# Kernel optimization log

Hardware: AMD Instinct MI355X
Metric: run time of the kernel (lower is better)

## Reference

```python
import jax, jax.numpy as jnp
import numpy as np

IN_FEATURES = 4096
OUT_FEATURES = 4096
N_GROUPS = 32
GROUP_SIZE = IN_FEATURES // N_GROUPS  # 128


def setup_inputs() -> dict:
    key = jax.random.key(0)
    k_x, k_qw, k_s, k_zp, k_b = jax.random.split(key, 5)
    x = jax.random.normal(k_x, (2, 2048, IN_FEATURES), dtype=jnp.float32)
    # 4-bit GPTQ quantized weight values in [0, 16)
    qweight_int = jax.random.randint(k_qw, (IN_FEATURES, OUT_FEATURES), 0, 16, dtype=jnp.int32)
    scales = jax.random.uniform(k_s, (N_GROUPS, OUT_FEATURES), dtype=jnp.float32, minval=0.001, maxval=0.02)
    zero_points = jax.random.randint(k_zp, (N_GROUPS, OUT_FEATURES), 0, 16, dtype=jnp.int32)
    # standard (non-permuted) g_idx: group index per input channel
    g_idx = (jnp.arange(IN_FEATURES, dtype=jnp.int32) // GROUP_SIZE).astype(jnp.int32)
    bias = jax.random.normal(k_b, (OUT_FEATURES,), dtype=jnp.float32)
    return {"x": x, "qweight_int": qweight_int, "scales": scales,
            "zero_points": zero_points, "g_idx": g_idx, "bias": bias}


def reference(x, qweight_int, scales, zero_points, g_idx, bias):
    dtype = x.dtype
    gi = g_idx.astype(jnp.int32)
    # dequantize: W[i, o] = scales[g_idx[i], o] * (q[i, o] - zp[g_idx[i], o])
    qw = qweight_int.astype(dtype)                       # [in, out]
    zp = zero_points.astype(dtype)[gi]                   # [in, out] via gather
    sc = scales.astype(dtype)[gi]                        # [in, out] via gather
    weight = sc * (qw - zp)                              # [in, out]
    out_shape = x.shape[:-1] + (qweight_int.shape[1],)
    x2d = x.reshape(-1, x.shape[-1])                     # [tokens, in]
    out = (x2d @ weight).reshape(out_shape)              # [b, s, out]
    out = out + bias.astype(dtype)
    return out
```

## Files before the change

### kernel.cpp

```cpp
#include <hip/hip_runtime.h>
#include <hip/hip_bf16.h>

typedef __hip_bfloat16 bf16;
typedef short short8 __attribute__((ext_vector_type(8)));
typedef float f32x4 __attribute__((ext_vector_type(4)));

#define M_DIM 4096
#define N_DIM 4096
#define K_DIM 4096

__global__ void prep_kernel(const float* __restrict__ x, bf16* __restrict__ xb,
                            const int* __restrict__ qw,
                            const float* __restrict__ scales,
                            const int* __restrict__ zps,
                            bf16* __restrict__ wt) {
    __shared__ bf16 t[64][72];
    const int tid = threadIdx.x;
    if (blockIdx.x < 16384) {
        int i = (blockIdx.x * 256 + tid) * 4;
        float4 v = *reinterpret_cast<const float4*>(x + i);
        union { bf16 b[4]; uint2 u; } o;
        o.b[0] = __float2bfloat16(v.x);
        o.b[1] = __float2bfloat16(v.y);
        o.b[2] = __float2bfloat16(v.z);
        o.b[3] = __float2bfloat16(v.w);
        *reinterpret_cast<uint2*>(xb + i) = o.u;
        return;
    }
    const int bx = blockIdx.x - 16384;
    const int n0 = (bx & 63) * 64;
    const int k0 = (bx >> 6) * 64;
    const int g  = k0 >> 7;
    const int tx = tid & 15, ty = tid >> 4;
    float sc[4], zp[4];
#pragma unroll
    for (int j = 0; j < 4; ++j) {
        int n = n0 + tx * 4 + j;
        sc[j] = scales[g * N_DIM + n];
        zp[j] = (float)zps[g * N_DIM + n];
    }
#pragma unroll
    for (int rr = 0; rr < 4; ++rr) {
        int row = ty + rr * 16;
        int4 q = *reinterpret_cast<const int4*>(qw + (long)(k0 + row) * N_DIM + n0 + tx * 4);
        t[tx * 4 + 0][row] = __float2bfloat16(sc[0] * ((float)q.x - zp[0]));
        t[tx * 4 + 1][row] = __float2bfloat16(sc[1] * ((float)q.y - zp[1]));
        t[tx * 4 + 2][row] = __float2bfloat16(sc[2] * ((float)q.z - zp[2]));
        t[tx * 4 + 3][row] = __float2bfloat16(sc[3] * ((float)q.w - zp[3]));
    }
    __syncthreads();
#pragma unroll
    for (int p = 0; p < 2; ++p) {
        int n  = (tid >> 3) + p * 32;
        int kc = (tid & 7) * 8;
        *reinterpret_cast<short8*>(wt + (long)(n0 + n) * K_DIM + k0 + kc) =
            *reinterpret_cast<const short8*>(&t[n][kc]);
    }
}

#define BM 256
#define BN 128
#define BK 64

__device__ __forceinline__ void async_ld16(const bf16* g, const bf16* l) {
    __builtin_amdgcn_global_load_lds(
        (const __attribute__((address_space(1))) void*)g,
        (__attribute__((address_space(3))) void*)l, 16, 0, 0);
}

__global__ __launch_bounds__(256, 2) void gemm_kernel(
    const bf16* __restrict__ A,
    const bf16* __restrict__ Bt,
    const float* __restrict__ bias,
    float* __restrict__ C) {
    __shared__ bf16 As[BM * BK];
    __shared__ bf16 Bs[BN * BK];
    const int tid  = threadIdx.x;
    const int wave = tid >> 6;
    const int lane = tid & 63;
    const int quad = lane >> 4;
    const int l16  = lane & 15;
    const int wm = (wave >> 1) * 128;
    const int wn = (wave & 1) * 64;
    const int m0 = blockIdx.y * BM;
    const int n0 = blockIdx.x * BN;

    const int srow  = tid >> 3;
    const int sunit = (tid & 7) ^ (srow & 7);
    const bf16* agp = A  + (long)(m0 + srow) * K_DIM + sunit * 8;
    const bf16* bgp = Bt + (long)(n0 + srow) * K_DIM + sunit * 8;
    const int ldsbase = wave * 512;

    f32x4 acc[8][4];
#pragma unroll
    for (int i = 0; i < 8; ++i)
#pragma unroll
        for (int j = 0; j < 4; ++j)
            acc[i][j] = {0.f, 0.f, 0.f, 0.f};

    for (int kk = 0; kk < K_DIM; kk += BK) {
#pragma unroll
        for (int i = 0; i < 8; ++i)
            async_ld16(agp + (long)i * 32 * K_DIM + kk, As + i * 2048 + ldsbase);
#pragma unroll
        for (int i = 0; i < 4; ++i)
            async_ld16(bgp + (long)i * 32 * K_DIM + kk, Bs + i * 2048 + ldsbase);
        __syncthreads();
#pragma unroll
        for (int ks = 0; ks < 2; ++ks) {
            short8 af[8], bfr[4];
#pragma unroll
            for (int mt = 0; mt < 8; ++mt) {
                int m = wm + mt * 16 + l16;
                int u = (ks * 4 + quad) ^ (m & 7);
                af[mt] = *reinterpret_cast<const short8*>(&As[m * 64 + u * 8]);
            }
#pragma unroll
            for (int nt = 0; nt < 4; ++nt) {
                int n = wn + nt * 16 + l16;
                int u = (ks * 4 + quad) ^ (n & 7);
                bfr[nt] = *reinterpret_cast<const short8*>(&Bs[n * 64 + u * 8]);
            }
#pragma unroll
            for (int mt = 0; mt < 8; ++mt)
#pragma unroll
                for (int nt = 0; nt < 4; ++nt)
                    acc[mt][nt] = __builtin_amdgcn_mfma_f32_16x16x32_bf16(
                        af[mt], bfr[nt], acc[mt][nt], 0, 0, 0);
        }
        __syncthreads();
    }

    float bv[4];
#pragma unroll
    for (int nt = 0; nt < 4; ++nt) bv[nt] = bias[n0 + wn + nt * 16 + l16];
#pragma unroll
    for (int mt = 0; mt < 8; ++mt) {
#pragma unroll
        for (int r = 0; r < 4; ++r) {
            int gm = m0 + wm + mt * 16 + quad * 4 + r;
            float* crow = C + (long)gm * N_DIM + n0 + wn;
#pragma unroll
            for (int nt = 0; nt < 4; ++nt)
                crow[nt * 16 + l16] = acc[mt][nt][r] + bv[nt];
        }
    }
}

extern "C" void kernel_launch(void* const* d_in, const int* in_sizes, int n_in,
                              void* d_out, int out_size, void* d_ws, size_t ws_size,
                              hipStream_t stream) {
    const float* x      = (const float*)d_in[0];
    const int*   qw     = (const int*)d_in[1];
    const float* scales = (const float*)d_in[2];
    const int*   zps    = (const int*)d_in[3];
    const float* bias   = (const float*)d_in[5];
    float* out = (float*)d_out;

    bf16* xb = (bf16*)d_ws;
    bf16* wt = (bf16*)((char*)d_ws + (size_t)M_DIM * K_DIM * 2);

    prep_kernel<<<16384 + 4096, 256, 0, stream>>>(x, xb, qw, scales, zps, wt);
    gemm_kernel<<<dim3(N_DIM / BN, M_DIM / BM), 256, 0, stream>>>(xb, wt, bias, out);
}
```

Measured before the change: 285.6 us.

## Switch GEMM to int8 MFMA with per-token activation quantization

Activations are quantized to int8 per row with an absmax scale, and weights are stored as int8 (q - zp) transposed. The GEMM uses 32x32x32 int8 MFMA with int32 partial sums per 128-wide group, then applies the group scale and the row scale in fp32. This halves operand bytes and uses the higher int8 matrix throughput. The cost is rounding error in the activations compared with the float reference, plus extra scaling work in the inner loop.

```diff
diff --git a/kernel.cpp b/kernel.cpp
--- a/kernel.cpp
+++ b/kernel.cpp
@@ -1,148 +1,198 @@
 #include <hip/hip_runtime.h>
 #include <hip/hip_bf16.h>
 
-typedef __hip_bfloat16 bf16;
-typedef short short8 __attribute__((ext_vector_type(8)));
-typedef float f32x4 __attribute__((ext_vector_type(4)));
+typedef int  int4v  __attribute__((ext_vector_type(4)));
+typedef int  int16v __attribute__((ext_vector_type(16)));
 
 #define M_DIM 4096
 #define N_DIM 4096
 #define K_DIM 4096
-
-__global__ void prep_kernel(const float* __restrict__ x, bf16* __restrict__ xb,
+#define NG 32
+#define GS 128
+
+__global__ void prep_kernel(const float* __restrict__ x,
+                            signed char* __restrict__ xq,
+                            float* __restrict__ sx,
                             const int* __restrict__ qw,
-                            const float* __restrict__ scales,
                             const int* __restrict__ zps,
-                            bf16* __restrict__ wt) {
-    __shared__ bf16 t[64][72];
+                            signed char* __restrict__ wq) {
+    __shared__ float red[4];
+    __shared__ float inv_s;
     const int tid = threadIdx.x;
-    if (blockIdx.x < 16384) {
-        int i = (blockIdx.x * 256 + tid) * 4;
-        float4 v = *reinterpret_cast<const float4*>(x + i);
-        union { bf16 b[4]; uint2 u; } o;
-        o.b[0] = __float2bfloat16(v.x);
-        o.b[1] = __float2bfloat16(v.y);
-        o.b[2] = __float2bfloat16(v.z);
-        o.b[3] = __float2bfloat16(v.w);
-        *reinterpret_cast<uint2*>(xb + i) = o.u;
+    if (blockIdx.x < 4096) {
+        const int m = blockIdx.x;
+        const float4* xr = reinterpret_cast<const float4*>(x + (long)m * K_DIM);
+        float4 v[4];
+        float amax = 0.f;
+#pragma unroll
+        for (int j = 0; j < 4; ++j) {
+            v[j] = xr[tid * 4 + j];
+            amax = fmaxf(amax, fmaxf(fmaxf(fabsf(v[j].x), fabsf(v[j].y)),
+                                     fmaxf(fabsf(v[j].z), fabsf(v[j].w))));
+        }
+#pragma unroll
+        for (int off = 32; off >= 1; off >>= 1)
+            amax = fmaxf(amax, __shfl_xor(amax, off));
+        if ((tid & 63) == 0) red[tid >> 6] = amax;
+        __syncthreads();
+        if (tid == 0) {
+            float a = fmaxf(fmaxf(red[0], red[1]), fmaxf(red[2], red[3]));
+            sx[m] = a * (1.f / 127.f);
+            inv_s = (a > 0.f) ? 127.f / a : 0.f;
+        }
+        __syncthreads();
+        const float inv = inv_s;
+        unsigned p[4];
+#pragma unroll
+        for (int j = 0; j < 4; ++j) {
+            int a0 = __float2int_rn(v[j].x * inv);
+            int a1 = __float2int_rn(v[j].y * inv);
+            int a2 = __float2int_rn(v[j].z * inv);
+            int a3 = __float2int_rn(v[j].w * inv);
+            p[j] = (a0 & 255) | ((a1 & 255) << 8) | ((a2 & 255) << 16) | ((a3 & 255) << 24);
+        }
+        *reinterpret_cast<uint4*>(xq + (long)m * K_DIM + tid * 16) =
+            make_uint4(p[0], p[1], p[2], p[3]);
         return;
     }
-    const int bx = blockIdx.x - 16384;
+    const int bx = blockIdx.x - 4096;
     const int n0 = (bx & 63) * 64;
     const int k0 = (bx >> 6) * 64;
     const int g  = k0 >> 7;
-    const int tx = tid & 15, ty = tid >> 4;
-    float sc[4], zp[4];
-#pragma unroll
-    for (int j = 0; j < 4; ++j) {
-        int n = n0 + tx * 4 + j;
-        sc[j] = scales[g * N_DIM + n];
-        zp[j] = (float)zps[g * N_DIM + n];
-    }
-#pragma unroll
-    for (int rr = 0; rr < 4; ++rr) {
-        int row = ty + rr * 16;
-        int4 q = *reinterpret_cast<const int4*>(qw + (long)(k0 + row) * N_DIM + n0 + tx * 4);
-        t[tx * 4 + 0][row] = __float2bfloat16(sc[0] * ((float)q.x - zp[0]));
-        t[tx * 4 + 1][row] = __float2bfloat16(sc[1] * ((float)q.y - zp[1]));
-        t[tx * 4 + 2][row] = __float2bfloat16(sc[2] * ((float)q.z - zp[2]));
-        t[tx * 4 + 3][row] = __float2bfloat16(sc[3] * ((float)q.w - zp[3]));
-    }
-    __syncthreads();
-#pragma unroll
-    for (int p = 0; p < 2; ++p) {
-        int n  = (tid >> 3) + p * 32;
-        int kc = (tid & 7) * 8;
-        *reinterpret_cast<short8*>(wt + (long)(n0 + n) * K_DIM + k0 + kc) =
-            *reinterpret_cast<const short8*>(&t[n][kc]);
-    }
+    const int n  = tid & 63;
+    const int w  = tid >> 6;
+    const int zp = zps[g * N_DIM + n0 + n];
+    const int kk = k0 + w * 16;
+    unsigned p[4];
+#pragma unroll
+    for (int c = 0; c < 4; ++c) {
+        unsigned acc = 0;
+#pragma unroll
+        for (int j = 0; j < 4; ++j) {
+            int q = qw[(long)(kk + c * 4 + j) * N_DIM + n0 + n];
+            acc |= (unsigned)((q - zp) & 255) << (8 * j);
+        }
+        p[c] = acc;
+    }
+    *reinterpret_cast<uint4*>(wq + (long)(n0 + n) * K_DIM + kk) =
+        make_uint4(p[0], p[1], p[2], p[3]);
 }
 
 #define BM 256
 #define BN 128
-#define BK 64
-
-__device__ __forceinline__ void async_ld16(const bf16* g, const bf16* l) {
+#define BK 128
+
+__device__ __forceinline__ void async_ld16(const signed char* g, const signed char* l) {
     __builtin_amdgcn_global_load_lds(
         (const __attribute__((address_space(1))) void*)g,
         (__attribute__((address_space(3))) void*)l, 16, 0, 0);
 }
 
 __global__ __launch_bounds__(256, 2) void gemm_kernel(
-    const bf16* __restrict__ A,
-    const bf16* __restrict__ Bt,
+    const signed char* __restrict__ A,
+    const signed char* __restrict__ Bq,
+    const float* __restrict__ scales,
+    const float* __restrict__ sx,
     const float* __restrict__ bias,
     float* __restrict__ C) {
-    __shared__ bf16 As[BM * BK];
-    __shared__ bf16 Bs[BN * BK];
+    __shared__ signed char As[BM * BK];
+    __shared__ signed char Bs[BN * BK];
+    __shared__ float sS[NG * BN];
+    __shared__ float sxs[BM];
     const int tid  = threadIdx.x;
     const int wave = tid >> 6;
     const int lane = tid & 63;
-    const int quad = lane >> 4;
-    const int l16  = lane & 15;
+    const int half = lane >> 5;
+    const int l32  = lane & 31;
     const int wm = (wave >> 1) * 128;
     const int wn = (wave & 1) * 64;
     const int m0 = blockIdx.y * BM;
     const int n0 = blockIdx.x * BN;
 
+#pragma unroll
+    for (int j = 0; j < 16; j += 4) {
+        int i = tid * 16 + j;
+        *reinterpret_cast<float4*>(&sS[i]) =
+            *reinterpret_cast<const float4*>(&scales[(i >> 7) * N_DIM + n0 + (i & 127)]);
+    }
+    sxs[tid] = sx[m0 + tid];
+
     const int srow  = tid >> 3;
     const int sunit = (tid & 7) ^ (srow & 7);
-    const bf16* agp = A  + (long)(m0 + srow) * K_DIM + sunit * 8;
-    const bf16* bgp = Bt + (long)(n0 + srow) * K_DIM + sunit * 8;
-    const int ldsbase = wave * 512;
-
-    f32x4 acc[8][4];
-#pragma unroll
-    for (int i = 0; i < 8; ++i)
-#pragma unroll
-        for (int j = 0; j < 4; ++j)
-            acc[i][j] = {0.f, 0.f, 0.f, 0.f};
+    const signed char* agp = A  + (long)(m0 + srow) * K_DIM + sunit * 16;
+    const signed char* bgp = Bq + (long)(n0 + srow) * K_DIM + sunit * 16;
+
+    float facc[4][2][16];
+#pragma unroll
+    for (int mt = 0; mt < 4; ++mt)
+#pragma unroll
+        for (int nt = 0; nt < 2; ++nt)
+#pragma unroll
+            for (int r = 0; r < 16; ++r) facc[mt][nt][r] = 0.f;
+    int16v zero16;
+#pragma unroll
+    for (int r = 0; r < 16; ++r) zero16[r] = 0;
 
     for (int kk = 0; kk < K_DIM; kk += BK) {
 #pragma unroll
-        for (int i = 0; i < 8; ++i)
-            async_ld16(agp + (long)i * 32 * K_DIM + kk, As + i * 2048 + ldsbase);
-#pragma unroll
-        for (int i = 0; i < 4; ++i)
-            async_ld16(bgp + (long)i * 32 * K_DIM + kk, Bs + i * 2048 + ldsbase);
-        __syncthreads();
-#pragma unroll
-        for (int ks = 0; ks < 2; ++ks) {
-            short8 af[8], bfr[4];
-#pragma unroll
-            for (int mt = 0; mt < 8; ++mt) {
-                int m = wm + mt * 16 + l16;
-                int u = (ks * 4 + quad) ^ (m & 7);
-                af[mt] = *reinterpret_cast<const short8*>(&As[m * 64 + u * 8]);
-            }
-#pragma unroll
-            for (int nt = 0; nt < 4; ++nt) {
-                int n = wn + nt * 16 + l16;
-                int u = (ks * 4 + quad) ^ (n & 7);
-                bfr[nt] = *reinterpret_cast<const short8*>(&Bs[n * 64 + u * 8]);
-            }
-#pragma unroll
-            for (int mt = 0; mt < 8; ++mt)
-#pragma unroll
-                for (int nt = 0; nt < 4; ++nt)
-                    acc[mt][nt] = __builtin_amdgcn_mfma_f32_16x16x32_bf16(
-                        af[mt], bfr[nt], acc[mt][nt], 0, 0, 0);
-        }
-        __syncthreads();
-    }
-
-    float bv[4];
-#pragma unroll
-    for (int nt = 0; nt < 4; ++nt) bv[nt] = bias[n0 + wn + nt * 16 + l16];
-#pragma unroll
-    for (int mt = 0; mt < 8; ++mt) {
-#pragma unroll
-        for (int r = 0; r < 4; ++r) {
-            int gm = m0 + wm + mt * 16 + quad * 4 + r;
+        for (int p = 0; p < 8; ++p)
+            async_ld16(agp + (long)p * 32 * K_DIM + kk, As + p * 4096 + wave * 1024);
+#pragma unroll
+        for (int p = 0; p < 4; ++p)
+            async_ld16(bgp + (long)p * 32 * K_DIM + kk, Bs + p * 4096 + wave * 1024);
+        __syncthreads();
+        const int g = kk >> 7;
+        const float s0 = sS[g * BN + wn + l32];
+        const float s1 = sS[g * BN + wn + 32 + l32];
+        int4v bf[2][4];
+#pragma unroll
+        for (int nt = 0; nt < 2; ++nt) {
+            int n = wn + nt * 32 + l32;
+#pragma unroll
+            for (int ks = 0; ks < 4; ++ks) {
+                int slot = (2 * ks + half) ^ (n & 7);
+                bf[nt][ks] = *reinterpret_cast<const int4v*>(&Bs[n * BK + slot * 16]);
+            }
+        }
+#pragma unroll
+        for (int mt = 0; mt < 4; ++mt) {
+            int m = wm + mt * 32 + l32;
+            int4v af[4];
+#pragma unroll
+            for (int ks = 0; ks < 4; ++ks) {
+                int slot = (2 * ks + half) ^ (m & 7);
+                af[ks] = *reinterpret_cast<const int4v*>(&As[m * BK + slot * 16]);
+            }
+            int16v c0 = __builtin_amdgcn_mfma_i32_32x32x32_i8(af[0], bf[0][0], zero16, 0, 0, 0);
+            int16v c1 = __builtin_amdgcn_mfma_i32_32x32x32_i8(af[0], bf[1][0], zero16, 0, 0, 0);
+#pragma unroll
+            for (int ks = 1; ks < 4; ++ks) {
+                c0 = __builtin_amdgcn_mfma_i32_32x32x32_i8(af[ks], bf[0][ks], c0, 0, 0, 0);
+                c1 = __builtin_amdgcn_mfma_i32_32x32x32_i8(af[ks], bf[1][ks], c1, 0, 0, 0);
+            }
+#pragma unroll
+            for (int r = 0; r < 16; ++r) {
+                facc[mt][0][r] += s0 * (float)c0[r];
+                facc[mt][1][r] += s1 * (float)c1[r];
+            }
+        }
+        __syncthreads();
+    }
+
+    float bv[2];
+    bv[0] = bias[n0 + wn + l32];
+    bv[1] = bias[n0 + wn + 32 + l32];
+    const int rowh = half * 4;
+#pragma unroll
+    for (int mt = 0; mt < 4; ++mt) {
+#pragma unroll
+        for (int r = 0; r < 16; ++r) {
+            int row = (r & 3) + 8 * (r >> 2) + rowh;
+            int gm  = m0 + wm + mt * 32 + row;
+            float sxm = sxs[wm + mt * 32 + row];
             float* crow = C + (long)gm * N_DIM + n0 + wn;
-#pragma unroll
-            for (int nt = 0; nt < 4; ++nt)
-                crow[nt * 16 + l16] = acc[mt][nt][r] + bv[nt];
+            crow[l32]      = facc[mt][0][r] * sxm + bv[0];
+            crow[32 + l32] = facc[mt][1][r] * sxm + bv[1];
         }
     }
 }
@@ -157,9 +207,11 @@
     const float* bias   = (const float*)d_in[5];
     float* out = (float*)d_out;
 
-    bf16* xb = (bf16*)d_ws;
-    bf16* wt = (bf16*)((char*)d_ws + (size_t)M_DIM * K_DIM * 2);
-
-    prep_kernel<<<16384 + 4096, 256, 0, stream>>>(x, xb, qw, scales, zps, wt);
-    gemm_kernel<<<dim3(N_DIM / BN, M_DIM / BM), 256, 0, stream>>>(xb, wt, bias, out);
-}
+    signed char* xq = (signed char*)d_ws;
+    signed char* wq = (signed char*)d_ws + (size_t)M_DIM * K_DIM;
+    float*       sx = (float*)((signed char*)d_ws + 2 * (size_t)M_DIM * K_DIM);
+
+    prep_kernel<<<8192, 256, 0, stream>>>(x, xq, sx, qw, zps, wq);
+    gemm_kernel<<<dim3(N_DIM / BN, M_DIM / BM), 256, 0, stream>>>(
+        xq, wq, scales, sx, bias, out);
+}
```

After: 265.0 us. 1.08x faster.
